# Performance work log

Hardware: AMD Instinct MI355X
Metric: run time of the kernel (lower is better)

The kernel has to match this reference:

```python
import jax, jax.numpy as jnp
import numpy as np

N_SRC = 100000   # source nodes
N_DST = 50000    # destination nodes
E = 600000       # edges (avg dst degree ~12)
D_IN = 128
D_OUT = 128


def setup_inputs() -> dict:
    key = jax.random.key(0)
    k1, k2, k3, k4 = jax.random.split(key, 4)
    H_src = jax.random.normal(k1, (N_SRC, D_IN), dtype=jnp.float32)
    edge_src = jax.random.randint(k2, (E,), 0, N_SRC)
    edge_dst = jax.random.randint(k3, (E,), 0, N_DST)
    # xavier_uniform-style scale for W
    limit = float(np.sqrt(6.0 / (D_IN + D_OUT)))
    W = jax.random.uniform(k4, (D_IN, D_OUT), dtype=jnp.float32, minval=-limit, maxval=limit)
    b = jnp.zeros((D_OUT,), dtype=jnp.float32)
    return {"H_src": H_src, "W": W, "b": b,
            "edge_src": edge_src, "edge_dst": edge_dst, "n_dst": N_DST}


def reference(H_src, W, b, edge_src, edge_dst, n_dst):
    # Linear transform: WH = H_src @ W + b        [N_src, D_OUT]
    WH = H_src @ W + b
    # Sparse aggregation: (A @ WH) as gather + segment_sum over edges
    agg = jax.ops.segment_sum(WH[edge_src], edge_dst, num_segments=n_dst)  # [N_dst, D_OUT]
    # Degree normalization: deg = row-sum of A, clamped to >= 1
    deg = jax.ops.segment_sum(jnp.ones(edge_dst.shape, WH.dtype), edge_dst,
                              num_segments=n_dst)
    deg = jnp.maximum(deg, 1.0)[:, None]
    return jax.nn.relu(agg / deg)
```

## Files before the change

kernel.cpp:

```cpp
#include <hip/hip_runtime.h>

#define D 128
#define LDA 136
#define BCAP 64
#define CSTRIDE 16
#define OVCAP 65536

typedef __attribute__((ext_vector_type(8))) short bf16x8;
typedef __attribute__((ext_vector_type(4))) float f32x4;
typedef __attribute__((ext_vector_type(4))) unsigned int u32x4;

static __device__ __forceinline__ unsigned short f2bf(float f) {
    unsigned u = __float_as_uint(f);
    unsigned r = 0x7fffu + ((u >> 16) & 1u);
    return (unsigned short)((u + r) >> 16);
}
static __device__ __forceinline__ float bflo(unsigned u) { return __uint_as_float(u << 16); }
static __device__ __forceinline__ float bfhi(unsigned u) { return __uint_as_float(u & 0xffff0000u); }

template<bool BF16H>
__global__ __launch_bounds__(256) void prep_kernel(
    const float* __restrict__ H, unsigned* __restrict__ Hb, int nh8,
    const float* __restrict__ W, unsigned short* __restrict__ Wt,
    const int* __restrict__ esrc, const int* __restrict__ edst, int E,
    int* __restrict__ counts, int* __restrict__ buckets,
    int* __restrict__ ovcnt, int* __restrict__ ovd, int* __restrict__ ovs)
{
    int i = blockIdx.x * 256 + threadIdx.x;

    int d = 0, s = 0, c = 0;
    bool hasE = (i < E);
    if (hasE) {
        d = __builtin_nontemporal_load(edst + i);
        s = __builtin_nontemporal_load(esrc + i);
    }
    if (hasE) c = atomicAdd(&counts[(size_t)d * CSTRIDE], 1);

    if (BF16H && i < nh8) {
        const f32x4* h4 = (const f32x4*)H;
        f32x4 v0 = __builtin_nontemporal_load(h4 + (size_t)i * 2);
        f32x4 v1 = __builtin_nontemporal_load(h4 + (size_t)i * 2 + 1);
        u32x4 o;
        o.x = (unsigned)f2bf(v0.x) | ((unsigned)f2bf(v0.y) << 16);
        o.y = (unsigned)f2bf(v0.z) | ((unsigned)f2bf(v0.w) << 16);
        o.z = (unsigned)f2bf(v1.x) | ((unsigned)f2bf(v1.y) << 16);
        o.w = (unsigned)f2bf(v1.z) | ((unsigned)f2bf(v1.w) << 16);
        __builtin_nontemporal_store(o, (u32x4*)Hb + i);
    } else {
        int j = i - nh8;
        if (j >= 0 && j < 16384) {
            int k = j >> 7, n = j & 127;
            float wv = __builtin_nontemporal_load(W + j);
            Wt[n * 128 + k] = f2bf(wv);
        }
    }

    if (hasE) {
        if (c < BCAP) {
            buckets[(size_t)d * BCAP + c] = s;
        } else {
            int o = atomicAdd(ovcnt, 1);
            if (o < OVCAP) { ovd[o] = d; ovs[o] = s; }
        }
    }
}

template<bool BF16H>
__global__ __launch_bounds__(256) void aggregate_kernel(
    const float* __restrict__ H, const uint4* __restrict__ Hb,
    const int* __restrict__ buckets, const int* __restrict__ counts,
    const int* __restrict__ ovcnt, const int* __restrict__ ovd,
    const int* __restrict__ ovs, unsigned short* __restrict__ aggb, int n_dst)
{
    int dst = blockIdx.x * 4 + (threadIdx.x >> 6);
    if (dst >= n_dst) return;
    int lane = threadIdx.x & 63;
    int dg = counts[(size_t)dst * CSTRIDE];
    int m = dg < BCAP ? dg : BCAP;
    int nov = *ovcnt; if (nov > OVCAP) nov = OVCAP;
    int idx = (lane < m) ? buckets[(size_t)dst * BCAP + lane] : 0;

    if (BF16H) {
        const int ql = lane & 15, quad = lane >> 4;
        float acc[8] = {0, 0, 0, 0, 0, 0, 0, 0};
        int j = 0;
        for (; j + 8 <= m; j += 8) {
            int sA = __shfl(idx, j + quad);
            int sB = __shfl(idx, j + 4 + quad);
            uint4 ha = Hb[(size_t)sA * 16 + ql];
            uint4 hb = Hb[(size_t)sB * 16 + ql];
            acc[0] += bflo(ha.x) + bflo(hb.x); acc[1] += bfhi(ha.x) + bfhi(hb.x);
            acc[2] += bflo(ha.y) + bflo(hb.y); acc[3] += bfhi(ha.y) + bfhi(hb.y);
            acc[4] += bflo(ha.z) + bflo(hb.z); acc[5] += bfhi(ha.z) + bfhi(hb.z);
            acc[6] += bflo(ha.w) + bflo(hb.w); acc[7] += bfhi(ha.w) + bfhi(hb.w);
        }
        for (; j < m; j += 4) {
            int jj = j + quad;
            int s = __shfl(idx, jj < m ? jj : m - 1);
            uint4 hv = Hb[(size_t)s * 16 + ql];
            float w = (jj < m) ? 1.f : 0.f;
            acc[0] += w * bflo(hv.x); acc[1] += w * bfhi(hv.x);
            acc[2] += w * bflo(hv.y); acc[3] += w * bfhi(hv.y);
            acc[4] += w * bflo(hv.z); acc[5] += w * bfhi(hv.z);
            acc[6] += w * bflo(hv.w); acc[7] += w * bfhi(hv.w);
        }
        for (int k = quad; k < nov; k += 4) {
            if (ovd[k] == dst) {
                uint4 hv = Hb[(size_t)ovs[k] * 16 + ql];
                acc[0] += bflo(hv.x); acc[1] += bfhi(hv.x);
                acc[2] += bflo(hv.y); acc[3] += bfhi(hv.y);
                acc[4] += bflo(hv.z); acc[5] += bfhi(hv.z);
                acc[6] += bflo(hv.w); acc[7] += bfhi(hv.w);
            }
        }
#pragma unroll
        for (int k = 0; k < 8; ++k) {
            acc[k] += __shfl_xor(acc[k], 16);
            acc[k] += __shfl_xor(acc[k], 32);
        }
        if (quad == 0) {
            uint4 o;
            o.x = (unsigned)f2bf(acc[0]) | ((unsigned)f2bf(acc[1]) << 16);
            o.y = (unsigned)f2bf(acc[2]) | ((unsigned)f2bf(acc[3]) << 16);
            o.z = (unsigned)f2bf(acc[4]) | ((unsigned)f2bf(acc[5]) << 16);
            o.w = (unsigned)f2bf(acc[6]) | ((unsigned)f2bf(acc[7]) << 16);
            ((uint4*)aggb)[(size_t)dst * 16 + ql] = o;
        }
    } else {
        const int hl = lane & 31, half = lane >> 5;
        const float4* H4 = (const float4*)H;
        float acc[4] = {0, 0, 0, 0};
        int j = 0;
        for (; j + 4 <= m; j += 4) {
            int sA = __shfl(idx, j + half);
            int sB = __shfl(idx, j + 2 + half);
            float4 va = H4[(size_t)sA * 32 + hl];
            float4 vb = H4[(size_t)sB * 32 + hl];
            acc[0] += va.x + vb.x; acc[1] += va.y + vb.y;
            acc[2] += va.z + vb.z; acc[3] += va.w + vb.w;
        }
        for (; j < m; j += 2) {
            int jj = j + half;
            int s = __shfl(idx, jj < m ? jj : m - 1);
            float4 v = H4[(size_t)s * 32 + hl];
            float w = (jj < m) ? 1.f : 0.f;
            acc[0] += w * v.x; acc[1] += w * v.y;
            acc[2] += w * v.z; acc[3] += w * v.w;
        }
        for (int k = half; k < nov; k += 2) {
            if (ovd[k] == dst) {
                float4 v = H4[(size_t)ovs[k] * 32 + hl];
                acc[0] += v.x; acc[1] += v.y; acc[2] += v.z; acc[3] += v.w;
            }
        }
#pragma unroll
        for (int k = 0; k < 4; ++k) acc[k] += __shfl_xor(acc[k], 32);
        if (half == 0) {
            uint2 o;
            o.x = (unsigned)f2bf(acc[0]) | ((unsigned)f2bf(acc[1]) << 16);
            o.y = (unsigned)f2bf(acc[2]) | ((unsigned)f2bf(acc[3]) << 16);
            ((uint2*)aggb)[(size_t)dst * 32 + hl] = o;
        }
    }
}

__global__ __launch_bounds__(256) void gemm_finalize_kernel(
    const unsigned short* __restrict__ aggb, const unsigned short* __restrict__ Wt,
    const float* __restrict__ b, const int* __restrict__ counts,
    float* __restrict__ out, int n_dst)
{
    __shared__ __align__(16) unsigned char smem[52224];
    unsigned short* Ash = (unsigned short*)smem;
    unsigned short* Wsh = (unsigned short*)(smem + 64 * LDA * 2);
    float* Csh = (float*)smem;

    const int tid  = threadIdx.x;
    const int lane = tid & 63, wv = tid >> 6;
    const size_t row0 = (size_t)blockIdx.x * 64;

#pragma unroll
    for (int t = 0; t < 4; ++t) {
        int i = tid + t * 256;
        int r = i >> 4, k8 = (i & 15) << 3;
        size_t gr = row0 + r;
        uint4 v = (gr < (size_t)n_dst) ? ((const uint4*)aggb)[gr * 16 + (i & 15)]
                                       : make_uint4(0, 0, 0, 0);
        *(uint4*)&Ash[r * LDA + k8] = v;
    }
#pragma unroll
    for (int t = 0; t < 8; ++t) {
        int i = tid + t * 256;
        int n = i >> 4, k8 = (i & 15) << 3;
        *(uint4*)&Wsh[n * LDA + k8] = ((const uint4*)Wt)[i];
    }
    __syncthreads();

    const int m0 = wv * 16;
    const int fl = lane & 15, quad = lane >> 4;

    f32x4 cacc[8];
#pragma unroll
    for (int n = 0; n < 8; ++n) cacc[n] = (f32x4){0.f, 0.f, 0.f, 0.f};

#pragma unroll
    for (int kc = 0; kc < 128; kc += 32) {
        bf16x8 a = *(const bf16x8*)&Ash[(m0 + fl) * LDA + kc + quad * 8];
#pragma unroll
        for (int n = 0; n < 8; ++n) {
            bf16x8 bf = *(const bf16x8*)&Wsh[(n * 16 + fl) * LDA + kc + quad * 8];
            cacc[n] = __builtin_amdgcn_mfma_f32_16x16x32_bf16(a, bf, cacc[n], 0, 0, 0);
        }
    }

    float inv[4], gate[4];
#pragma unroll
    for (int r = 0; r < 4; ++r) {
        size_t gr = row0 + m0 + quad * 4 + r;
        int dg = (gr < (size_t)n_dst) ? counts[gr * CSTRIDE] : 0;
        inv[r]  = 1.0f / (float)(dg > 1 ? dg : 1);
        gate[r] = (dg > 0) ? 1.0f : 0.0f;
    }
    __syncthreads();

#pragma unroll
    for (int n = 0; n < 8; ++n) {
        int col = n * 16 + fl;
        float bc = b[col];
#pragma unroll
        for (int r = 0; r < 4; ++r) {
            float v = cacc[n][r] * inv[r] + bc * gate[r];
            Csh[(m0 + quad * 4 + r) * 132 + col] = fmaxf(v, 0.0f);
        }
    }
    __syncthreads();

#pragma unroll
    for (int t = 0; t < 8; ++t) {
        int i = tid + t * 256;
        int rr = i >> 5, c4 = i & 31;
        size_t gr = row0 + rr;
        if (gr < (size_t)n_dst) {
            f32x4 vout = *(f32x4*)&Csh[rr * 132 + c4 * 4];
            __builtin_nontemporal_store(vout, (f32x4*)out + gr * (D / 4) + c4);
        }
    }
}

extern "C" void kernel_launch(void* const* d_in, const int* in_sizes, int n_in,
                              void* d_out, int out_size, void* d_ws, size_t ws_size,
                              hipStream_t stream) {
    const float* H    = (const float*)d_in[0];
    const float* W    = (const float*)d_in[1];
    const float* b    = (const float*)d_in[2];
    const int*   esrc = (const int*)d_in[3];
    const int*   edst = (const int*)d_in[4];
    const int    E     = in_sizes[3];
    const int    n_dst = out_size / D;
    const int    nsrc_elems = in_sizes[0];

    float* out = (float*)d_out;

    char* p = (char*)d_ws;
    unsigned short* Wt = (unsigned short*)p;  p += 128 * 128 * sizeof(unsigned short);
    int* counts = (int*)p;  p += (size_t)n_dst * CSTRIDE * 4;
    int* ovcnt  = (int*)p;  p += 256;
    int* ovd    = (int*)p;  p += (size_t)OVCAP * 4;
    int* ovs    = (int*)p;  p += (size_t)OVCAP * 4;
    int* buckets= (int*)p;  p += (size_t)n_dst * BCAP * 4;
    size_t agg_off = (((size_t)(p - (char*)d_ws)) + 255) & ~(size_t)255;
    unsigned short* aggb = (unsigned short*)((char*)d_ws + agg_off);
    size_t hb_off = (agg_off + (size_t)n_dst * D * 2 + 255) & ~(size_t)255;
    bool use_bf16h = (ws_size >= hb_off + (size_t)nsrc_elems * 2);
    unsigned* Hb = (unsigned*)((char*)d_ws + hb_off);

    const int nh8 = use_bf16h ? nsrc_elems / 8 : 0;
    int prep_work = nh8 + 16384;
    if (prep_work < E) prep_work = E;

    hipMemsetAsync(counts, 0, (size_t)n_dst * CSTRIDE * 4 + 256, stream);

    if (use_bf16h) {
        prep_kernel<true><<<(prep_work + 255) / 256, 256, 0, stream>>>(
            H, Hb, nh8, W, Wt, esrc, edst, E, counts, buckets, ovcnt, ovd, ovs);
        aggregate_kernel<true><<<(n_dst + 3) / 4, 256, 0, stream>>>(
            H, (const uint4*)Hb, buckets, counts, ovcnt, ovd, ovs, aggb, n_dst);
    } else {
        prep_kernel<false><<<(prep_work + 255) / 256, 256, 0, stream>>>(
            H, Hb, nh8, W, Wt, esrc, edst, E, counts, buckets, ovcnt, ovd, ovs);
        aggregate_kernel<false><<<(n_dst + 3) / 4, 256, 0, stream>>>(
            H, nullptr, buckets, counts, ovcnt, ovd, ovs, aggb, n_dst);
    }

    gemm_finalize_kernel<<<(n_dst + 63) / 64, 256, 0, stream>>>(
        aggb, Wt, b, counts, out, n_dst);
}
```

Measured before the change: 169.6 us.

## Fuse neighbor aggregation into GEMM finalize kernel to skip aggregate round-trip

On the bf16 path, aggregation and the MFMA GEMM/normalize/ReLU stage are merged into one kernel. Each block aggregates 64 destination rows into shared memory, with each wave handling 16 rows in sequence and prefetching the next row's bucket indices, then runs the GEMM directly from shared memory. This removes the global bf16 agg buffer write and read and one kernel launch. In exchange, gather parallelism per block drops: each wave now walks 16 rows serially instead of one row per wave across many blocks. Fewer blocks are resident because of the shared memory footprint, which may expose gather latency.

After: 193.9 us. 1.14x slower.

```diff
diff --git a/kernel.cpp b/kernel.cpp
--- a/kernel.cpp
+++ b/kernel.cpp
@@ -65,9 +65,151 @@
     }
 }
 
-template<bool BF16H>
-__global__ __launch_bounds__(256) void aggregate_kernel(
-    const float* __restrict__ H, const uint4* __restrict__ Hb,
+__global__ __launch_bounds__(256) void fused_agg_gemm_kernel(
+    const uint4* __restrict__ Hb, const int* __restrict__ buckets,
+    const int* __restrict__ counts, const int* __restrict__ ovcnt,
+    const int* __restrict__ ovd, const int* __restrict__ ovs,
+    const unsigned short* __restrict__ Wt, const float* __restrict__ b,
+    float* __restrict__ out, int n_dst)
+{
+    __shared__ __align__(16) unsigned char smem[52224];
+    unsigned short* Ash = (unsigned short*)smem;
+    unsigned short* Wsh = (unsigned short*)(smem + 64 * LDA * 2);
+    float* Csh = (float*)smem;
+
+    const int tid  = threadIdx.x;
+    const int lane = tid & 63, wv = tid >> 6;
+    const size_t row0 = (size_t)blockIdx.x * 64;
+    const int ql = lane & 15, quad = lane >> 4;
+
+#pragma unroll
+    for (int t = 0; t < 8; ++t) {
+        int i = tid + t * 256;
+        int n = i >> 4, k8 = (i & 15) << 3;
+        *(uint4*)&Wsh[n * LDA + k8] = ((const uint4*)Wt)[i];
+    }
+
+    int nov = *ovcnt; if (nov > OVCAP) nov = OVCAP;
+
+    const int dst0 = (int)row0 + wv * 16;
+    int dgv = 0;
+    if (lane < 16 && dst0 + lane < n_dst)
+        dgv = counts[(size_t)(dst0 + lane) * CSTRIDE];
+
+    int m_cur = __shfl(dgv, 0); m_cur = m_cur < BCAP ? m_cur : BCAP;
+    int idx_cur = (lane < m_cur) ? buckets[(size_t)dst0 * BCAP + lane] : 0;
+
+    for (int r = 0; r < 16; ++r) {
+        int m_next = 0, idx_next = 0;
+        if (r + 1 < 16) {
+            m_next = __shfl(dgv, r + 1); m_next = m_next < BCAP ? m_next : BCAP;
+            idx_next = (lane < m_next) ? buckets[(size_t)(dst0 + r + 1) * BCAP + lane] : 0;
+        }
+        int m = m_cur, idx = idx_cur, dst = dst0 + r;
+
+        float acc[8] = {0, 0, 0, 0, 0, 0, 0, 0};
+        int j = 0;
+        for (; j + 8 <= m; j += 8) {
+            int sA = __shfl(idx, j + quad);
+            int sB = __shfl(idx, j + 4 + quad);
+            uint4 ha = Hb[(size_t)sA * 16 + ql];
+            uint4 hb = Hb[(size_t)sB * 16 + ql];
+            acc[0] += bflo(ha.x) + bflo(hb.x); acc[1] += bfhi(ha.x) + bfhi(hb.x);
+            acc[2] += bflo(ha.y) + bflo(hb.y); acc[3] += bfhi(ha.y) + bfhi(hb.y);
+            acc[4] += bflo(ha.z) + bflo(hb.z); acc[5] += bfhi(ha.z) + bfhi(hb.z);
+            acc[6] += bflo(ha.w) + bflo(hb.w); acc[7] += bfhi(ha.w) + bfhi(hb.w);
+        }
+        for (; j < m; j += 4) {
+            int jj = j + quad;
+            int s = __shfl(idx, jj < m ? jj : m - 1);
+            uint4 hv = Hb[(size_t)s * 16 + ql];
+            float w = (jj < m) ? 1.f : 0.f;
+            acc[0] += w * bflo(hv.x); acc[1] += w * bfhi(hv.x);
+            acc[2] += w * bflo(hv.y); acc[3] += w * bfhi(hv.y);
+            acc[4] += w * bflo(hv.z); acc[5] += w * bfhi(hv.z);
+            acc[6] += w * bflo(hv.w); acc[7] += w * bfhi(hv.w);
+        }
+        if (dst < n_dst) {
+            for (int k = quad; k < nov; k += 4) {
+                if (ovd[k] == dst) {
+                    uint4 hv = Hb[(size_t)ovs[k] * 16 + ql];
+                    acc[0] += bflo(hv.x); acc[1] += bfhi(hv.x);
+                    acc[2] += bflo(hv.y); acc[3] += bfhi(hv.y);
+                    acc[4] += bflo(hv.z); acc[5] += bfhi(hv.z);
+                    acc[6] += bflo(hv.w); acc[7] += bfhi(hv.w);
+                }
+            }
+        }
+#pragma unroll
+        for (int k = 0; k < 8; ++k) {
+            acc[k] += __shfl_xor(acc[k], 16);
+            acc[k] += __shfl_xor(acc[k], 32);
+        }
+        if (quad == 0) {
+            uint4 o;
+            o.x = (unsigned)f2bf(acc[0]) | ((unsigned)f2bf(acc[1]) << 16);
+            o.y = (unsigned)f2bf(acc[2]) | ((unsigned)f2bf(acc[3]) << 16);
+            o.z = (unsigned)f2bf(acc[4]) | ((unsigned)f2bf(acc[5]) << 16);
+            o.w = (unsigned)f2bf(acc[6]) | ((unsigned)f2bf(acc[7]) << 16);
+            *(uint4*)&Ash[(wv * 16 + r) * LDA + ql * 8] = o;
+        }
+        m_cur = m_next; idx_cur = idx_next;
+    }
+    __syncthreads();
+
+    const int m0 = wv * 16;
+    const int fl = lane & 15;
+
+    f32x4 cacc[8];
+#pragma unroll
+    for (int n = 0; n < 8; ++n) cacc[n] = (f32x4){0.f, 0.f, 0.f, 0.f};
+
+#pragma unroll
+    for (int kc = 0; kc < 128; kc += 32) {
+        bf16x8 a = *(const bf16x8*)&Ash[(m0 + fl) * LDA + kc + quad * 8];
+#pragma unroll
+        for (int n = 0; n < 8; ++n) {
+            bf16x8 bf = *(const bf16x8*)&Wsh[(n * 16 + fl) * LDA + kc + quad * 8];
+            cacc[n] = __builtin_amdgcn_mfma_f32_16x16x32_bf16(a, bf, cacc[n], 0, 0, 0);
+        }
+    }
+
+    float inv[4], gate[4];
+#pragma unroll
+    for (int r = 0; r < 4; ++r) {
+        size_t gr = row0 + m0 + quad * 4 + r;
+        int dg = (gr < (size_t)n_dst) ? counts[gr * CSTRIDE] : 0;
+        inv[r]  = 1.0f / (float)(dg > 1 ? dg : 1);
+        gate[r] = (dg > 0) ? 1.0f : 0.0f;
+    }
+    __syncthreads();
+
+#pragma unroll
+    for (int n = 0; n < 8; ++n) {
+        int col = n * 16 + fl;
+        float bc = b[col];
+#pragma unroll
+        for (int r = 0; r < 4; ++r) {
+            float v = cacc[n][r] * inv[r] + bc * gate[r];
+            Csh[(m0 + quad * 4 + r) * 132 + col] = fmaxf(v, 0.0f);
+        }
+    }
+    __syncthreads();
+
+#pragma unroll
+    for (int t = 0; t < 8; ++t) {
+        int i = tid + t * 256;
+        int rr = i >> 5, c4 = i & 31;
+        size_t gr = row0 + rr;
+        if (gr < (size_t)n_dst) {
+            f32x4 vout = *(f32x4*)&Csh[rr * 132 + c4 * 4];
+            __builtin_nontemporal_store(vout, (f32x4*)out + gr * (D / 4) + c4);
+        }
+    }
+}
+
+__global__ __launch_bounds__(256) void aggregate_kernel_f32(
+    const float* __restrict__ H,
     const int* __restrict__ buckets, const int* __restrict__ counts,
     const int* __restrict__ ovcnt, const int* __restrict__ ovd,
     const int* __restrict__ ovs, unsigned short* __restrict__ aggb, int n_dst)
@@ -80,87 +222,39 @@
     int nov = *ovcnt; if (nov > OVCAP) nov = OVCAP;
     int idx = (lane < m) ? buckets[(size_t)dst * BCAP + lane] : 0;
 
-    if (BF16H) {
-        const int ql = lane & 15, quad = lane >> 4;
-        float acc[8] = {0, 0, 0, 0, 0, 0, 0, 0};
-        int j = 0;
-        for (; j + 8 <= m; j += 8) {
-            int sA = __shfl(idx, j + quad);
-            int sB = __shfl(idx, j + 4 + quad);
-            uint4 ha = Hb[(size_t)sA * 16 + ql];
-            uint4 hb = Hb[(size_t)sB * 16 + ql];
-            acc[0] += bflo(ha.x) + bflo(hb.x); acc[1] += bfhi(ha.x) + bfhi(hb.x);
-            acc[2] += bflo(ha.y) + bflo(hb.y); acc[3] += bfhi(ha.y) + bfhi(hb.y);
-            acc[4] += bflo(ha.z) + bflo(hb.z); acc[5] += bfhi(ha.z) + bfhi(hb.z);
-            acc[6] += bflo(ha.w) + bflo(hb.w); acc[7] += bfhi(ha.w) + bfhi(hb.w);
-        }
-        for (; j < m; j += 4) {
-            int jj = j + quad;
-            int s = __shfl(idx, jj < m ? jj : m - 1);
-            uint4 hv = Hb[(size_t)s * 16 + ql];
-            float w = (jj < m) ? 1.f : 0.f;
-            acc[0] += w * bflo(hv.x); acc[1] += w * bfhi(hv.x);
-            acc[2] += w * bflo(hv.y); acc[3] += w * bfhi(hv.y);
-            acc[4] += w * bflo(hv.z); acc[5] += w * bfhi(hv.z);
-            acc[6] += w * bflo(hv.w); acc[7] += w * bfhi(hv.w);
-        }
-        for (int k = quad; k < nov; k += 4) {
-            if (ovd[k] == dst) {
-                uint4 hv = Hb[(size_t)ovs[k] * 16 + ql];
-                acc[0] += bflo(hv.x); acc[1] += bfhi(hv.x);
-                acc[2] += bflo(hv.y); acc[3] += bfhi(hv.y);
-                acc[4] += bflo(hv.z); acc[5] += bfhi(hv.z);
-                acc[6] += bflo(hv.w); acc[7] += bfhi(hv.w);
-            }
-        }
-#pragma unroll
-        for (int k = 0; k < 8; ++k) {
-            acc[k] += __shfl_xor(acc[k], 16);
-            acc[k] += __shfl_xor(acc[k], 32);
-        }
-        if (quad == 0) {
-            uint4 o;
-            o.x = (unsigned)f2bf(acc[0]) | ((unsigned)f2bf(acc[1]) << 16);
-            o.y = (unsigned)f2bf(acc[2]) | ((unsigned)f2bf(acc[3]) << 16);
-            o.z = (unsigned)f2bf(acc[4]) | ((unsigned)f2bf(acc[5]) << 16);
-            o.w = (unsigned)f2bf(acc[6]) | ((unsigned)f2bf(acc[7]) << 16);
-            ((uint4*)aggb)[(size_t)dst * 16 + ql] = o;
-        }
-    } else {
-        const int hl = lane & 31, half = lane >> 5;
-        const float4* H4 = (const float4*)H;
-        float acc[4] = {0, 0, 0, 0};
-        int j = 0;
-        for (; j + 4 <= m; j += 4) {
-            int sA = __shfl(idx, j + half);
-            int sB = __shfl(idx, j + 2 + half);
-            float4 va = H4[(size_t)sA * 32 + hl];
-            float4 vb = H4[(size_t)sB * 32 + hl];
-            acc[0] += va.x + vb.x; acc[1] += va.y + vb.y;
-            acc[2] += va.z + vb.z; acc[3] += va.w + vb.w;
-        }
-        for (; j < m; j += 2) {
-            int jj = j + half;
-            int s = __shfl(idx, jj < m ? jj : m - 1);
-            float4 v = H4[(size_t)s * 32 + hl];
-            float w = (jj < m) ? 1.f : 0.f;
-            acc[0] += w * v.x; acc[1] += w * v.y;
-            acc[2] += w * v.z; acc[3] += w * v.w;
-        }
-        for (int k = half; k < nov; k += 2) {
-            if (ovd[k] == dst) {
-                float4 v = H4[(size_t)ovs[k] * 32 + hl];
-                acc[0] += v.x; acc[1] += v.y; acc[2] += v.z; acc[3] += v.w;
-            }
-        }
-#pragma unroll
-        for (int k = 0; k < 4; ++k) acc[k] += __shfl_xor(acc[k], 32);
-        if (half == 0) {
-            uint2 o;
-            o.x = (unsigned)f2bf(acc[0]) | ((unsigned)f2bf(acc[1]) << 16);
-            o.y = (unsigned)f2bf(acc[2]) | ((unsigned)f2bf(acc[3]) << 16);
-            ((uint2*)aggb)[(size_t)dst * 32 + hl] = o;
-        }
+    const int hl = lane & 31, half = lane >> 5;
+    const float4* H4 = (const float4*)H;
+    float acc[4] = {0, 0, 0, 0};
+    int j = 0;
+    for (; j + 4 <= m; j += 4) {
+        int sA = __shfl(idx, j + half);
+        int sB = __shfl(idx, j + 2 + half);
+        float4 va = H4[(size_t)sA * 32 + hl];
+        float4 vb = H4[(size_t)sB * 32 + hl];
+        acc[0] += va.x + vb.x; acc[1] += va.y + vb.y;
+        acc[2] += va.z + vb.z; acc[3] += va.w + vb.w;
+    }
+    for (; j < m; j += 2) {
+        int jj = j + half;
+        int s = __shfl(idx, jj < m ? jj : m - 1);
+        float4 v = H4[(size_t)s * 32 + hl];
+        float w = (jj < m) ? 1.f : 0.f;
+        acc[0] += w * v.x; acc[1] += w * v.y;
+        acc[2] += w * v.z; acc[3] += w * v.w;
+    }
+    for (int k = half; k < nov; k += 2) {
+        if (ovd[k] == dst) {
+            float4 v = H4[(size_t)ovs[k] * 32 + hl];
+            acc[0] += v.x; acc[1] += v.y; acc[2] += v.z; acc[3] += v.w;
+        }
+    }
+#pragma unroll
+    for (int k = 0; k < 4; ++k) acc[k] += __shfl_xor(acc[k], 32);
+    if (half == 0) {
+        uint2 o;
+        o.x = (unsigned)f2bf(acc[0]) | ((unsigned)f2bf(acc[1]) << 16);
+        o.y = (unsigned)f2bf(acc[2]) | ((unsigned)f2bf(acc[3]) << 16);
+        ((uint2*)aggb)[(size_t)dst * 32 + hl] = o;
     }
 }
 
@@ -282,15 +376,14 @@
     if (use_bf16h) {
         prep_kernel<true><<<(prep_work + 255) / 256, 256, 0, stream>>>(
             H, Hb, nh8, W, Wt, esrc, edst, E, counts, buckets, ovcnt, ovd, ovs);
-        aggregate_kernel<true><<<(n_dst + 3) / 4, 256, 0, stream>>>(
-            H, (const uint4*)Hb, buckets, counts, ovcnt, ovd, ovs, aggb, n_dst);
+        fused_agg_gemm_kernel<<<(n_dst + 63) / 64, 256, 0, stream>>>(
+            (const uint4*)Hb, buckets, counts, ovcnt, ovd, ovs, Wt, b, out, n_dst);
     } else {
         prep_kernel<false><<<(prep_work + 255) / 256, 256, 0, stream>>>(
             H, Hb, nh8, W, Wt, esrc, edst, E, counts, buckets, ovcnt, ovd, ovs);
-        aggregate_kernel<false><<<(n_dst + 3) / 4, 256, 0, stream>>>(
-            H, nullptr, buckets, counts, ovcnt, ovd, ovs, aggb, n_dst);
-    }
-
-    gemm_finalize_kernel<<<(n_dst + 63) / 64, 256, 0, stream>>>(
-        aggb, Wt, b, counts, out, n_dst);
-}
+        aggregate_kernel_f32<<<(n_dst + 3) / 4, 256, 0, stream>>>(
+            H, buckets, counts, ovcnt, ovd, ovs, aggb, n_dst);
+        gemm_finalize_kernel<<<(n_dst + 63) / 64, 256, 0, stream>>>(
+            aggb, Wt, b, counts, out, n_dst);
+    }
+}
```

## Reorder to GEMM-then-aggregate, fusing H transform into prep and finalize into gather

Applied to the files above, without the earlier changes.

The computation order changes from aggregate-then-GEMM to GEMM-on-sources-then-aggregate. The prep kernel now computes WH = H@W in bf16 with MFMA while it also bins the edges. The aggregation kernel gathers WH rows and applies bias, degree normalization and ReLU directly, which removes the separate GEMM/finalize kernel and the bf16 agg round trip. The cost is a GEMM over twice as many rows (100k sources instead of 50k destinations), and the edge bucketing now shares a kernel with MFMA work.

Measured after the change: 171.9 us. About the same (+1.4%).

```diff
diff --git a/kernel.cpp b/kernel.cpp
--- a/kernel.cpp
+++ b/kernel.cpp
@@ -18,56 +18,223 @@
 static __device__ __forceinline__ float bflo(unsigned u) { return __uint_as_float(u << 16); }
 static __device__ __forceinline__ float bfhi(unsigned u) { return __uint_as_float(u & 0xffff0000u); }
 
-template<bool BF16H>
-__global__ __launch_bounds__(256) void prep_kernel(
-    const float* __restrict__ H, unsigned* __restrict__ Hb, int nh8,
+__global__ __launch_bounds__(256, 4) void prep_gemm_kernel(
+    const float* __restrict__ H, int n_src, const float* __restrict__ W,
+    unsigned short* __restrict__ WHb,
+    const int* __restrict__ esrc, const int* __restrict__ edst, int E,
+    int* __restrict__ counts, int* __restrict__ buckets,
+    int* __restrict__ ovcnt, int* __restrict__ ovd, int* __restrict__ ovs)
+{
+    __shared__ __align__(16) unsigned char smem[34816];
+    unsigned short* Wsh = (unsigned short*)smem;
+    float* Csh = (float*)smem;
+
+    const int tid = threadIdx.x, bid = blockIdx.x;
+    const int gt = (int)gridDim.x * 256;
+
+    int e0 = bid * 256 + tid, e1 = e0 + gt;
+    bool h0 = (e0 < E), h1 = (e1 < E);
+    int d0 = 0, s0 = 0, d1 = 0, s1 = 0, c0 = 0, c1 = 0;
+    if (h0) { d0 = __builtin_nontemporal_load(edst + e0);
+              s0 = __builtin_nontemporal_load(esrc + e0); }
+    if (h1) { d1 = __builtin_nontemporal_load(edst + e1);
+              s1 = __builtin_nontemporal_load(esrc + e1); }
+    if (h0) c0 = atomicAdd(&counts[(size_t)d0 * CSTRIDE], 1);
+    if (h1) c1 = atomicAdd(&counts[(size_t)d1 * CSTRIDE], 1);
+
+    const f32x4* W4 = (const f32x4*)W;
+#pragma unroll
+    for (int t = 0; t < 16; ++t) {
+        int i4 = tid + t * 256;
+        f32x4 w = W4[i4];
+        int ib = i4 * 4;
+        Wsh[((ib + 0) & 127) * LDA + ((ib + 0) >> 7)] = f2bf(w.x);
+        Wsh[((ib + 1) & 127) * LDA + ((ib + 1) >> 7)] = f2bf(w.y);
+        Wsh[((ib + 2) & 127) * LDA + ((ib + 2) >> 7)] = f2bf(w.z);
+        Wsh[((ib + 3) & 127) * LDA + ((ib + 3) >> 7)] = f2bf(w.w);
+    }
+    __syncthreads();
+
+    const int lane = tid & 63, wvid = tid >> 6;
+    const int fl = lane & 15, quad = lane >> 4;
+    const int rowbase = bid * 64;
+    const bool doG = (rowbase < n_src);
+
+    f32x4 cacc[8];
+#pragma unroll
+    for (int n = 0; n < 8; ++n) cacc[n] = (f32x4){0.f, 0.f, 0.f, 0.f};
+
+    if (doG) {
+        int arow = rowbase + wvid * 16 + fl;
+        bool rok = (arow < n_src);
+        const f32x4* H4 = (const f32x4*)H;
+        size_t base = (size_t)arow * 32 + quad * 2;
+        f32x4 z = (f32x4){0.f, 0.f, 0.f, 0.f};
+        f32x4 av0 = rok ? H4[base +  0] : z, av1 = rok ? H4[base +  1] : z;
+        f32x4 av2 = rok ? H4[base +  8] : z, av3 = rok ? H4[base +  9] : z;
+        f32x4 av4 = rok ? H4[base + 16] : z, av5 = rok ? H4[base + 17] : z;
+        f32x4 av6 = rok ? H4[base + 24] : z, av7 = rok ? H4[base + 25] : z;
+
+#define PACK_A(a, v0, v1)                                                    \
+        { a[0] = (short)f2bf(v0.x); a[1] = (short)f2bf(v0.y);                \
+          a[2] = (short)f2bf(v0.z); a[3] = (short)f2bf(v0.w);                \
+          a[4] = (short)f2bf(v1.x); a[5] = (short)f2bf(v1.y);                \
+          a[6] = (short)f2bf(v1.z); a[7] = (short)f2bf(v1.w); }
+#define MSTEP(a, KC)                                                          \
+        _Pragma("unroll")                                                     \
+        for (int n = 0; n < 8; ++n) {                                         \
+            bf16x8 bf = *(const bf16x8*)&Wsh[(n * 16 + fl) * LDA + (KC) + quad * 8]; \
+            cacc[n] = __builtin_amdgcn_mfma_f32_16x16x32_bf16(a, bf, cacc[n], 0, 0, 0); \
+        }
+        bf16x8 a0, a1, a2, a3;
+        PACK_A(a0, av0, av1) PACK_A(a1, av2, av3)
+        PACK_A(a2, av4, av5) PACK_A(a3, av6, av7)
+        MSTEP(a0, 0) MSTEP(a1, 32) MSTEP(a2, 64) MSTEP(a3, 96)
+#undef PACK_A
+#undef MSTEP
+    }
+    __syncthreads();
+
+    if (doG) {
+#pragma unroll
+        for (int n = 0; n < 8; ++n) {
+            int col = n * 16 + fl;
+#pragma unroll
+            for (int r = 0; r < 4; ++r)
+                Csh[(wvid * 16 + quad * 4 + r) * 132 + col] = cacc[n][r];
+        }
+    }
+    __syncthreads();
+
+    if (doG) {
+#pragma unroll
+        for (int t = 0; t < 4; ++t) {
+            int i = tid + t * 256;
+            int rr = i >> 4, cu = i & 15;
+            size_t gr = (size_t)rowbase + rr;
+            if (gr < (size_t)n_src) {
+                float* s = &Csh[rr * 132 + cu * 8];
+                f32x4 lo = *(f32x4*)s, hi = *(f32x4*)(s + 4);
+                u32x4 o;
+                o.x = (unsigned)f2bf(lo.x) | ((unsigned)f2bf(lo.y) << 16);
+                o.y = (unsigned)f2bf(lo.z) | ((unsigned)f2bf(lo.w) << 16);
+                o.z = (unsigned)f2bf(hi.x) | ((unsigned)f2bf(hi.y) << 16);
+                o.w = (unsigned)f2bf(hi.z) | ((unsigned)f2bf(hi.w) << 16);
+                ((u32x4*)WHb)[gr * 16 + cu] = o;
+            }
+        }
+    }
+
+    if (h0) {
+        if (c0 < BCAP) buckets[(size_t)d0 * BCAP + c0] = s0;
+        else { int o = atomicAdd(ovcnt, 1); if (o < OVCAP) { ovd[o] = d0; ovs[o] = s0; } }
+    }
+    if (h1) {
+        if (c1 < BCAP) buckets[(size_t)d1 * BCAP + c1] = s1;
+        else { int o = atomicAdd(ovcnt, 1); if (o < OVCAP) { ovd[o] = d1; ovs[o] = s1; } }
+    }
+    for (int e = e0 + 2 * gt; e < E; e += gt) {
+        int dd = edst[e], ss = esrc[e];
+        int cc = atomicAdd(&counts[(size_t)dd * CSTRIDE], 1);
+        if (cc < BCAP) buckets[(size_t)dd * BCAP + cc] = ss;
+        else { int o = atomicAdd(ovcnt, 1); if (o < OVCAP) { ovd[o] = dd; ovs[o] = ss; } }
+    }
+}
+
+__global__ __launch_bounds__(256) void agg_finalize_kernel(
+    const uint4* __restrict__ WHb, const int* __restrict__ buckets,
+    const int* __restrict__ counts, const int* __restrict__ ovcnt,
+    const int* __restrict__ ovd, const int* __restrict__ ovs,
+    const float* __restrict__ b, float* __restrict__ out, int n_dst)
+{
+    int dst = blockIdx.x * 4 + (threadIdx.x >> 6);
+    if (dst >= n_dst) return;
+    int lane = threadIdx.x & 63;
+    int dg = counts[(size_t)dst * CSTRIDE];
+    int m = dg < BCAP ? dg : BCAP;
+    int nov = *ovcnt; if (nov > OVCAP) nov = OVCAP;
+    int idx = (lane < m) ? buckets[(size_t)dst * BCAP + lane] : 0;
+
+    const int ql = lane & 15, quad = lane >> 4;
+    float acc[8] = {0, 0, 0, 0, 0, 0, 0, 0};
+    int j = 0;
+    for (; j + 8 <= m; j += 8) {
+        int sA = __shfl(idx, j + quad);
+        int sB = __shfl(idx, j + 4 + quad);
+        uint4 ha = WHb[(size_t)sA * 16 + ql];
+        uint4 hb = WHb[(size_t)sB * 16 + ql];
+        acc[0] += bflo(ha.x) + bflo(hb.x); acc[1] += bfhi(ha.x) + bfhi(hb.x);
+        acc[2] += bflo(ha.y) + bflo(hb.y); acc[3] += bfhi(ha.y) + bfhi(hb.y);
+        acc[4] += bflo(ha.z) + bflo(hb.z); acc[5] += bfhi(ha.z) + bfhi(hb.z);
+        acc[6] += bflo(ha.w) + bflo(hb.w); acc[7] += bfhi(ha.w) + bfhi(hb.w);
+    }
+    for (; j < m; j += 4) {
+        int jj = j + quad;
+        int s = __shfl(idx, jj < m ? jj : m - 1);
+        uint4 hv = WHb[(size_t)s * 16 + ql];
+        float w = (jj < m) ? 1.f : 0.f;
+        acc[0] += w * bflo(hv.x); acc[1] += w * bfhi(hv.x);
+        acc[2] += w * bflo(hv.y); acc[3] += w * bfhi(hv.y);
+        acc[4] += w * bflo(hv.z); acc[5] += w * bfhi(hv.z);
+        acc[6] += w * bflo(hv.w); acc[7] += w * bfhi(hv.w);
+    }
+    for (int k = quad; k < nov; k += 4) {
+        if (ovd[k] == dst) {
+            uint4 hv = WHb[(size_t)ovs[k] * 16 + ql];
+            acc[0] += bflo(hv.x); acc[1] += bfhi(hv.x);
+            acc[2] += bflo(hv.y); acc[3] += bfhi(hv.y);
+            acc[4] += bflo(hv.z); acc[5] += bfhi(hv.z);
+            acc[6] += bflo(hv.w); acc[7] += bfhi(hv.w);
+        }
+    }
+#pragma unroll
+    for (int k = 0; k < 8; ++k) {
+        acc[k] += __shfl_xor(acc[k], 16);
+        acc[k] += __shfl_xor(acc[k], 32);
+    }
+    if (quad == 0) {
+        float inv  = 1.0f / (float)(dg > 1 ? dg : 1);
+        float gate = (dg > 0) ? 1.0f : 0.0f;
+        const f32x4* b4 = (const f32x4*)b;
+        f32x4 b0 = b4[ql * 2], b1 = b4[ql * 2 + 1];
+        f32x4 o0, o1;
+        o0.x = fmaxf(acc[0] * inv + b0.x * gate, 0.f);
+        o0.y = fmaxf(acc[1] * inv + b0.y * gate, 0.f);
+        o0.z = fmaxf(acc[2] * inv + b0.z * gate, 0.f);
+        o0.w = fmaxf(acc[3] * inv + b0.w * gate, 0.f);
+        o1.x = fmaxf(acc[4] * inv + b1.x * gate, 0.f);
+        o1.y = fmaxf(acc[5] * inv + b1.y * gate, 0.f);
+        o1.z = fmaxf(acc[6] * inv + b1.z * gate, 0.f);
+        o1.w = fmaxf(acc[7] * inv + b1.w * gate, 0.f);
+        f32x4* op = (f32x4*)out + (size_t)dst * 32 + ql * 2;
+        __builtin_nontemporal_store(o0, op);
+        __builtin_nontemporal_store(o1, op + 1);
+    }
+}
+
+__global__ __launch_bounds__(256) void prep_fb_kernel(
     const float* __restrict__ W, unsigned short* __restrict__ Wt,
     const int* __restrict__ esrc, const int* __restrict__ edst, int E,
     int* __restrict__ counts, int* __restrict__ buckets,
     int* __restrict__ ovcnt, int* __restrict__ ovd, int* __restrict__ ovs)
 {
     int i = blockIdx.x * 256 + threadIdx.x;
-
     int d = 0, s = 0, c = 0;
     bool hasE = (i < E);
+    if (hasE) { d = edst[i]; s = esrc[i]; }
+    if (hasE) c = atomicAdd(&counts[(size_t)d * CSTRIDE], 1);
+    if (i < 16384) {
+        int k = i >> 7, n = i & 127;
+        Wt[n * 128 + k] = f2bf(W[i]);
+    }
     if (hasE) {
-        d = __builtin_nontemporal_load(edst + i);
-        s = __builtin_nontemporal_load(esrc + i);
-    }
-    if (hasE) c = atomicAdd(&counts[(size_t)d * CSTRIDE], 1);
-
-    if (BF16H && i < nh8) {
-        const f32x4* h4 = (const f32x4*)H;
-        f32x4 v0 = __builtin_nontemporal_load(h4 + (size_t)i * 2);
-        f32x4 v1 = __builtin_nontemporal_load(h4 + (size_t)i * 2 + 1);
-        u32x4 o;
-        o.x = (unsigned)f2bf(v0.x) | ((unsigned)f2bf(v0.y) << 16);
-        o.y = (unsigned)f2bf(v0.z) | ((unsigned)f2bf(v0.w) << 16);
-        o.z = (unsigned)f2bf(v1.x) | ((unsigned)f2bf(v1.y) << 16);
-        o.w = (unsigned)f2bf(v1.z) | ((unsigned)f2bf(v1.w) << 16);
-        __builtin_nontemporal_store(o, (u32x4*)Hb + i);
-    } else {
-        int j = i - nh8;
-        if (j >= 0 && j < 16384) {
-            int k = j >> 7, n = j & 127;
-            float wv = __builtin_nontemporal_load(W + j);
-            Wt[n * 128 + k] = f2bf(wv);
-        }
-    }
-
-    if (hasE) {
-        if (c < BCAP) {
-            buckets[(size_t)d * BCAP + c] = s;
-        } else {
-            int o = atomicAdd(ovcnt, 1);
-            if (o < OVCAP) { ovd[o] = d; ovs[o] = s; }
-        }
-    }
-}
-
-template<bool BF16H>
-__global__ __launch_bounds__(256) void aggregate_kernel(
-    const float* __restrict__ H, const uint4* __restrict__ Hb,
+        if (c < BCAP) buckets[(size_t)d * BCAP + c] = s;
+        else { int o = atomicAdd(ovcnt, 1); if (o < OVCAP) { ovd[o] = d; ovs[o] = s; } }
+    }
+}
+
+__global__ __launch_bounds__(256) void aggregate_kernel_f32(
+    const float* __restrict__ H,
     const int* __restrict__ buckets, const int* __restrict__ counts,
     const int* __restrict__ ovcnt, const int* __restrict__ ovd,
     const int* __restrict__ ovs, unsigned short* __restrict__ aggb, int n_dst)
@@ -80,87 +247,39 @@
     int nov = *ovcnt; if (nov > OVCAP) nov = OVCAP;
     int idx = (lane < m) ? buckets[(size_t)dst * BCAP + lane] : 0;
 
-    if (BF16H) {
-        const int ql = lane & 15, quad = lane >> 4;
-        float acc[8] = {0, 0, 0, 0, 0, 0, 0, 0};
-        int j = 0;
-        for (; j + 8 <= m; j += 8) {
-            int sA = __shfl(idx, j + quad);
-            int sB = __shfl(idx, j + 4 + quad);
-            uint4 ha = Hb[(size_t)sA * 16 + ql];
-            uint4 hb = Hb[(size_t)sB * 16 + ql];
-            acc[0] += bflo(ha.x) + bflo(hb.x); acc[1] += bfhi(ha.x) + bfhi(hb.x);
-            acc[2] += bflo(ha.y) + bflo(hb.y); acc[3] += bfhi(ha.y) + bfhi(hb.y);
-            acc[4] += bflo(ha.z) + bflo(hb.z); acc[5] += bfhi(ha.z) + bfhi(hb.z);
-            acc[6] += bflo(ha.w) + bflo(hb.w); acc[7] += bfhi(ha.w) + bfhi(hb.w);
-        }
-        for (; j < m; j += 4) {
-            int jj = j + quad;
-            int s = __shfl(idx, jj < m ? jj : m - 1);
-            uint4 hv = Hb[(size_t)s * 16 + ql];
-            float w = (jj < m) ? 1.f : 0.f;
-            acc[0] += w * bflo(hv.x); acc[1] += w * bfhi(hv.x);
-            acc[2] += w * bflo(hv.y); acc[3] += w * bfhi(hv.y);
-            acc[4] += w * bflo(hv.z); acc[5] += w * bfhi(hv.z);
-            acc[6] += w * bflo(hv.w); acc[7] += w * bfhi(hv.w);
-        }
-        for (int k = quad; k < nov; k += 4) {
-            if (ovd[k] == dst) {
-                uint4 hv = Hb[(size_t)ovs[k] * 16 + ql];
-                acc[0] += bflo(hv.x); acc[1] += bfhi(hv.x);
-                acc[2] += bflo(hv.y); acc[3] += bfhi(hv.y);
-                acc[4] += bflo(hv.z); acc[5] += bfhi(hv.z);
-                acc[6] += bflo(hv.w); acc[7] += bfhi(hv.w);
-            }
-        }
-#pragma unroll
-        for (int k = 0; k < 8; ++k) {
-            acc[k] += __shfl_xor(acc[k], 16);
-            acc[k] += __shfl_xor(acc[k], 32);
-        }
-        if (quad == 0) {
-            uint4 o;
-            o.x = (unsigned)f2bf(acc[0]) | ((unsigned)f2bf(acc[1]) << 16);
-            o.y = (unsigned)f2bf(acc[2]) | ((unsigned)f2bf(acc[3]) << 16);
-            o.z = (unsigned)f2bf(acc[4]) | ((unsigned)f2bf(acc[5]) << 16);
-            o.w = (unsigned)f2bf(acc[6]) | ((unsigned)f2bf(acc[7]) << 16);
-            ((uint4*)aggb)[(size_t)dst * 16 + ql] = o;
-        }
-    } else {
-        const int hl = lane & 31, half = lane >> 5;
-        const float4* H4 = (const float4*)H;
-        float acc[4] = {0, 0, 0, 0};
-        int j = 0;
-        for (; j + 4 <= m; j += 4) {
-            int sA = __shfl(idx, j + half);
-            int sB = __shfl(idx, j + 2 + half);
-            float4 va = H4[(size_t)sA * 32 + hl];
-            float4 vb = H4[(size_t)sB * 32 + hl];
-            acc[0] += va.x + vb.x; acc[1] += va.y + vb.y;
-            acc[2] += va.z + vb.z; acc[3] += va.w + vb.w;
-        }
-        for (; j < m; j += 2) {
-            int jj = j + half;
-            int s = __shfl(idx, jj < m ? jj : m - 1);
-            float4 v = H4[(size_t)s * 32 + hl];
-            float w = (jj < m) ? 1.f : 0.f;
-            acc[0] += w * v.x; acc[1] += w * v.y;
-            acc[2] += w * v.z; acc[3] += w * v.w;
-        }
-        for (int k = half; k < nov; k += 2) {
-            if (ovd[k] == dst) {
-                float4 v = H4[(size_t)ovs[k] * 32 + hl];
-                acc[0] += v.x; acc[1] += v.y; acc[2] += v.z; acc[3] += v.w;
-            }
-        }
-#pragma unroll
-        for (int k = 0; k < 4; ++k) acc[k] += __shfl_xor(acc[k], 32);
-        if (half == 0) {
-            uint2 o;
-            o.x = (unsigned)f2bf(acc[0]) | ((unsigned)f2bf(acc[1]) << 16);
-            o.y = (unsigned)f2bf(acc[2]) | ((unsigned)f2bf(acc[3]) << 16);
-            ((uint2*)aggb)[(size_t)dst * 32 + hl] = o;
-        }
+    const int hl = lane & 31, half = lane >> 5;
+    const float4* H4 = (const float4*)H;
+    float acc[4] = {0, 0, 0, 0};
+    int j = 0;
+    for (; j + 4 <= m; j += 4) {
+        int sA = __shfl(idx, j + half);
+        int sB = __shfl(idx, j + 2 + half);
+        float4 va = H4[(size_t)sA * 32 + hl];
+        float4 vb = H4[(size_t)sB * 32 + hl];
+        acc[0] += va.x + vb.x; acc[1] += va.y + vb.y;
+        acc[2] += va.z + vb.z; acc[3] += va.w + vb.w;
+    }
+    for (; j < m; j += 2) {
+        int jj = j + half;
+        int s = __shfl(idx, jj < m ? jj : m - 1);
+        float4 v = H4[(size_t)s * 32 + hl];
+        float w = (jj < m) ? 1.f : 0.f;
+        acc[0] += w * v.x; acc[1] += w * v.y;
+        acc[2] += w * v.z; acc[3] += w * v.w;
+    }
+    for (int k = half; k < nov; k += 2) {
+        if (ovd[k] == dst) {
+            float4 v = H4[(size_t)ovs[k] * 32 + hl];
+            acc[0] += v.x; acc[1] += v.y; acc[2] += v.z; acc[3] += v.w;
+        }
+    }
+#pragma unroll
+    for (int k = 0; k < 4; ++k) acc[k] += __shfl_xor(acc[k], 32);
+    if (half == 0) {
+        uint2 o;
+        o.x = (unsigned)f2bf(acc[0]) | ((unsigned)f2bf(acc[1]) << 16);
+        o.y = (unsigned)f2bf(acc[2]) | ((unsigned)f2bf(acc[3]) << 16);
+        ((uint2*)aggb)[(size_t)dst * 32 + hl] = o;
     }
 }
 
@@ -257,6 +376,7 @@
     const int    E     = in_sizes[3];
     const int    n_dst = out_size / D;
     const int    nsrc_elems = in_sizes[0];
+    const int    n_src = nsrc_elems / D;
 
     float* out = (float*)d_out;
 
@@ -269,28 +389,27 @@
     int* buckets= (int*)p;  p += (size_t)n_dst * BCAP * 4;
     size_t agg_off = (((size_t)(p - (char*)d_ws)) + 255) & ~(size_t)255;
     unsigned short* aggb = (unsigned short*)((char*)d_ws + agg_off);
-    size_t hb_off = (agg_off + (size_t)n_dst * D * 2 + 255) & ~(size_t)255;
-    bool use_bf16h = (ws_size >= hb_off + (size_t)nsrc_elems * 2);
-    unsigned* Hb = (unsigned*)((char*)d_ws + hb_off);
-
-    const int nh8 = use_bf16h ? nsrc_elems / 8 : 0;
-    int prep_work = nh8 + 16384;
-    if (prep_work < E) prep_work = E;
+    size_t wh_off = (agg_off + (size_t)n_dst * D * 2 + 255) & ~(size_t)255;
+    bool use_wh = (ws_size >= wh_off + (size_t)nsrc_elems * 2);
+    unsigned short* WHb = (unsigned short*)((char*)d_ws + wh_off);
 
     hipMemsetAsync(counts, 0, (size_t)n_dst * CSTRIDE * 4 + 256, stream);
 
-    if (use_bf16h) {
-        prep_kernel<true><<<(prep_work + 255) / 256, 256, 0, stream>>>(
-            H, Hb, nh8, W, Wt, esrc, edst, E, counts, buckets, ovcnt, ovd, ovs);
-        aggregate_kernel<true><<<(n_dst + 3) / 4, 256, 0, stream>>>(
-            H, (const uint4*)Hb, buckets, counts, ovcnt, ovd, ovs, aggb, n_dst);
+    if (use_wh) {
+        int G = (n_src + 63) / 64;
+        int Ge = (E + 511) / 512;
+        if (Ge > G) G = Ge;
+        prep_gemm_kernel<<<G, 256, 0, stream>>>(
+            H, n_src, W, WHb, esrc, edst, E, counts, buckets, ovcnt, ovd, ovs);
+        agg_finalize_kernel<<<(n_dst + 3) / 4, 256, 0, stream>>>(
+            (const uint4*)WHb, buckets, counts, ovcnt, ovd, ovs, b, out, n_dst);
     } else {
-        prep_kernel<false><<<(prep_work + 255) / 256, 256, 0, stream>>>(
-            H, Hb, nh8, W, Wt, esrc, edst, E, counts, buckets, ovcnt, ovd, ovs);
-        aggregate_kernel<false><<<(n_dst + 3) / 4, 256, 0, stream>>>(
-            H, nullptr, buckets, counts, ovcnt, ovd, ovs, aggb, n_dst);
-    }
-
-    gemm_finalize_kernel<<<(n_dst + 63) / 64, 256, 0, stream>>>(
-        aggb, Wt, b, counts, out, n_dst);
-}
+        int prep_work = E > 16384 ? E : 16384;
+        prep_fb_kernel<<<(prep_work + 255) / 256, 256, 0, stream>>>(
+            W, Wt, esrc, edst, E, counts, buckets, ovcnt, ovd, ovs);
+        aggregate_kernel_f32<<<(n_dst + 3) / 4, 256, 0, stream>>>(
+            H, buckets, counts, ovcnt, ovd, ovs, aggb, n_dst);
+        gemm_finalize_kernel<<<(n_dst + 63) / 64, 256, 0, stream>>>(
+            aggb, Wt, b, counts, out, n_dst);
+    }
+}
```
